# Kernel optimization log

Measured on AMD Instinct MI355X. Metric: run time of the kernel, lower is better.

## Reference

```python
import jax, jax.numpy as jnp
import numpy as np

D_MODEL = 512
NUM_HEADS = 8
HEAD_DIM = D_MODEL // NUM_HEADS
NUM_RBF = 16
MAX_DIST = 2.0
SCALE = HEAD_DIM ** -0.5
SIGMA = MAX_DIST / NUM_RBF


def setup_inputs() -> dict:
    key = jax.random.key(0)
    ks = jax.random.split(key, 8)
    B, L = 4, 1024
    x = jax.random.normal(ks[0], (B, L, D_MODEL), dtype=jnp.float32)
    coords = jax.random.normal(ks[1], (B, L, 3), dtype=jnp.float32)
    mask = jnp.ones((B, L), dtype=bool)
    # torch Linear weights stored transposed: (in, out)
    s = 1.0 / np.sqrt(D_MODEL)
    Wqkv = jax.random.uniform(ks[2], (D_MODEL, 3 * D_MODEL), jnp.float32, -s, s)
    bqkv = jax.random.uniform(ks[3], (3 * D_MODEL,), jnp.float32, -s, s)
    sr = 1.0 / np.sqrt(NUM_RBF)
    Wbias = jax.random.uniform(ks[4], (NUM_RBF, NUM_HEADS), jnp.float32, -sr, sr)
    bbias = jax.random.uniform(ks[5], (NUM_HEADS,), jnp.float32, -sr, sr)
    Wout = jax.random.uniform(ks[6], (D_MODEL, D_MODEL), jnp.float32, -s, s)
    bout = jax.random.uniform(ks[7], (D_MODEL,), jnp.float32, -s, s)
    return {"x": x, "coords": coords, "mask": mask,
            "Wqkv": Wqkv, "bqkv": bqkv, "Wbias": Wbias, "bbias": bbias,
            "Wout": Wout, "bout": bout}


def reference(x, coords, mask, Wqkv, bqkv, Wbias, bbias, Wout, bout):
    B, L, _ = x.shape
    qkv = x @ Wqkv + bqkv                              # (B,L,3*d)
    qkv = qkv.reshape(B, L, 3, NUM_HEADS, HEAD_DIM)
    qkv = jnp.transpose(qkv, (2, 0, 3, 1, 4))          # (3,B,H,L,hd)
    q, k, v = qkv[0], qkv[1], qkv[2]
    logits = jnp.einsum('bhqd,bhkd->bhqk', q, k) * SCALE
    # pairwise euclidean distances with safe sqrt (zero grad at d=0)
    diff = coords[:, :, None, :] - coords[:, None, :, :]  # (B,L,L,3)
    d2 = jnp.sum(diff * diff, axis=-1)
    dists = jnp.where(d2 > 0, jnp.sqrt(jnp.where(d2 > 0, d2, 1.0)), 0.0)
    mu = jnp.linspace(0.0, MAX_DIST, NUM_RBF)
    rbf = jnp.exp(-(dists[..., None] - mu) ** 2 / (2.0 * SIGMA ** 2))  # (B,L,L,R)
    geo = rbf @ Wbias + bbias                          # (B,L,L,H)
    logits = logits + jnp.transpose(geo, (0, 3, 1, 2))  # (B,H,L,L)
    neg_inf = jnp.finfo(logits.dtype).min
    logits = jnp.where(mask[:, None, None, :], logits, neg_inf)
    w = jax.nn.softmax(logits, axis=-1)
    out = jnp.einsum('bhqk,bhkd->bhqd', w, v)
    out = jnp.transpose(out, (0, 2, 1, 3)).reshape(B, L, D_MODEL)
    return out @ Wout + bout
```

## Files before the change

kernel.cpp:

```cpp
#include <hip/hip_runtime.h>
#include <hip/hip_bf16.h>

typedef unsigned short u16;
typedef unsigned int   u32;
typedef __attribute__((ext_vector_type(8))) __bf16 bf16x8;
typedef __attribute__((ext_vector_type(8))) unsigned short u16x8;
typedef __attribute__((ext_vector_type(4))) float  f32x4;

#define LOG2E 1.4426950408889634f
#define SC2   (0.125f * LOG2E)
#define NTAB  512
#define INV_DT128 21802.667f

__device__ __forceinline__ u16 f2bf(float f) {
  u32 u = __float_as_uint(f);
  u32 r = (u + 0x7FFFu + ((u >> 16) & 1u)) >> 16;
  return (u16)r;
}

__device__ __forceinline__ void gld16(const void* g, void* l) {
  __builtin_amdgcn_global_load_lds((const __attribute__((address_space(1))) void*)g,
                                   (__attribute__((address_space(3))) void*)l,
                                   16, 0, 0);
}

__device__ __forceinline__ int sigma64(int l) {
  return (l & ~0x3C) | ((l >> 2) & 0x0C) | ((l << 2) & 0x30);
}

__device__ __forceinline__ void tr64_body(const float* __restrict__ in, u16* __restrict__ out,
                                          int R, int C, int c0, int r0, int tid,
                                          float (*tile)[65]) {
  const int cl = tid & 63, rl = tid >> 6;
#pragma unroll
  for (int p = 0; p < 16; ++p) {
    int row = p * 4 + rl;
    tile[row][cl] = in[(size_t)(r0 + row) * C + c0 + cl];
  }
  __syncthreads();
#pragma unroll
  for (int p = 0; p < 16; ++p) {
    int cc = p * 4 + rl;
    out[(size_t)(c0 + cc) * R + r0 + cl] = f2bf(tile[cl][cc]);
  }
}

__global__ __launch_bounds__(256) void prep(
    const float* __restrict__ x, const float* __restrict__ Wqkv, const float* __restrict__ Wout,
    const float* __restrict__ Wbias, const float* __restrict__ bbias,
    const float* __restrict__ coords,
    u16* __restrict__ xb, u16* __restrict__ wqkvT, u16* __restrict__ woutT,
    u32* __restrict__ gpack, u16* __restrict__ didx) {
  __shared__ float tile[64][65];
  const int bx = blockIdx.x, tid = threadIdx.x;
  if (bx < 2048) {
    int i = bx * 256 + tid;
    float4 v = ((const float4*)x)[i];
    ushort4 o;
    o.x = f2bf(v.x); o.y = f2bf(v.y); o.z = f2bf(v.z); o.w = f2bf(v.w);
    ((ushort4*)xb)[i] = o;
  } else if (bx < 2240) {
    int t = bx - 2048;
    tr64_body(Wqkv, wqkvT, 512, 1536, (t % 24) * 64, (t / 24) * 64, tid, tile);
  } else if (bx < 2304) {
    int t = bx - 2240;
    tr64_body(Wout, woutT, 512, 512, (t & 7) * 64, (t >> 3) * 64, tid, tile);
  } else if (bx < 2306) {
    int i = (bx - 2304) * 256 + tid;
    float d0 = (float)i * (3.0f / 511.0f);
    float d1 = (float)(i + 1) * (3.0f / 511.0f);
    float g0[8], g1[8];
#pragma unroll
    for (int h = 0; h < 8; ++h) { g0[h] = bbias[h]; g1[h] = bbias[h]; }
#pragma unroll
    for (int r = 0; r < 16; ++r) {
      float mu = (float)r * (2.0f / 15.0f);
      float e0 = __expf(-(d0 - mu) * (d0 - mu) * 32.0f);
      float e1 = __expf(-(d1 - mu) * (d1 - mu) * 32.0f);
#pragma unroll
      for (int h = 0; h < 8; ++h) {
        g0[h] += e0 * Wbias[r * 8 + h];
        g1[h] += e1 * Wbias[r * 8 + h];
      }
    }
#pragma unroll
    for (int h = 0; h < 8; ++h) {
      u32 lo = f2bf(g0[h] * LOG2E);
      u32 hi = f2bf((g1[h] - g0[h]) * (LOG2E / 128.0f));
      gpack[h * NTAB + i] = (hi << 16) | lo;
    }
  } else {
    __shared__ float rcf[12];
    int bi = bx - 2306;
    int b = bi >> 8, it = bi & 255;
    int i0 = it * 4;
    if (tid < 12) rcf[tid] = coords[(size_t)b * 3072 + i0 * 3 + tid];
    __syncthreads();
#pragma unroll
    for (int jt = 0; jt < 4; ++jt) {
      int j = jt * 256 + tid;
      float cx = coords[((size_t)b * 1024 + j) * 3 + 0];
      float cy = coords[((size_t)b * 1024 + j) * 3 + 1];
      float cz = coords[((size_t)b * 1024 + j) * 3 + 2];
#pragma unroll
      for (int ii = 0; ii < 4; ++ii) {
        float dx = rcf[ii * 3 + 0] - cx, dy = rcf[ii * 3 + 1] - cy, dz = rcf[ii * 3 + 2] - cz;
        float d = sqrtf(fmaf(dx, dx, fmaf(dy, dy, dz * dz)));
        float t = fminf(d * INV_DT128, 65407.0f);
        didx[((size_t)b << 20) + (size_t)(i0 + ii) * 1024 + j] = (u16)(t + 0.5f);
      }
    }
  }
}

template <int EPI, int NT, int MT>
__global__ __launch_bounds__(256) void gemm_bt(
    const u16* __restrict__ A, const u16* __restrict__ Bt, const float* __restrict__ bias,
    float* __restrict__ Cf, u16* __restrict__ Qb, u16* __restrict__ Kb, u16* __restrict__ Vt,
    int N, int K) {
  __shared__ __attribute__((aligned(16))) u16 As[MT * 64 * 64];
  __shared__ __attribute__((aligned(16))) u16 Bs[NT * 16 * 64];
  const int tid = threadIdx.x;
  const int w = tid >> 6, lane = tid & 63;
  const int lm = lane & 15, lg = lane >> 4;
  const int m0 = blockIdx.y * (MT * 64), n0 = blockIdx.x * (NT * 16);
  const f32x4 z4 = {0.f, 0.f, 0.f, 0.f};
  f32x4 acc[MT][NT];
#pragma unroll
  for (int mt = 0; mt < MT; ++mt)
#pragma unroll
    for (int nt = 0; nt < NT; ++nt) acc[mt][nt] = z4;

  for (int k0 = 0; k0 < K; k0 += 64) {
    __syncthreads();
#pragma unroll
    for (int j = 0; j < 2 * MT; ++j) {
      int cidx = j * 256 + tid;
      int row = cidx >> 3, c8 = cidx & 7;
      gld16(A + (size_t)(m0 + row) * K + k0 + c8 * 8, &As[cidx * 8]);
    }
#pragma unroll
    for (int j = 0; j < NT / 2; ++j) {
      int cidx = j * 256 + tid;
      int row = cidx >> 3, c8 = cidx & 7;
      gld16(Bt + (size_t)(n0 + row) * K + k0 + c8 * 8, &Bs[cidx * 8]);
    }
    __syncthreads();
#pragma unroll
    for (int c = 0; c < 2; ++c) {
      const int ko = c * 32 + lg * 8;
      bf16x8 af[MT], bfr[NT];
#pragma unroll
      for (int mt = 0; mt < MT; ++mt)
        af[mt] = *(const bf16x8*)&As[(w * (MT * 16) + mt * 16 + lm) * 64 + ko];
#pragma unroll
      for (int nt = 0; nt < NT; ++nt)
        bfr[nt] = *(const bf16x8*)&Bs[(nt * 16 + lm) * 64 + ko];
#pragma unroll
      for (int mt = 0; mt < MT; ++mt)
#pragma unroll
        for (int nt = 0; nt < NT; ++nt)
          acc[mt][nt] = __builtin_amdgcn_mfma_f32_16x16x32_bf16(af[mt], bfr[nt], acc[mt][nt], 0, 0, 0);
    }
  }

#pragma unroll
  for (int mt = 0; mt < MT; ++mt) {
#pragma unroll
    for (int nt = 0; nt < NT; ++nt) {
      const int n = n0 + nt * 16 + lm;
      const float bv = bias[n];
#pragma unroll
      for (int r = 0; r < 4; ++r) {
        const int m = m0 + w * (MT * 16) + mt * 16 + lg * 4 + r;
        float v = acc[mt][nt][r] + bv;
        if (EPI == 1) {
          Cf[(size_t)m * N + n] = v;
        } else {
          int b = m >> 10, l = m & 1023;
          int which = n >> 9, f = n & 511, h = f >> 6, o = f & 63;
          u16 hv = f2bf(v);
          int lp = (l & ~63) | sigma64(l & 63);
          if (which == 0)      Qb[(((size_t)(b * 8 + h)) * 1024 + l) * 64 + o] = hv;
          else if (which == 1) Kb[(((size_t)(b * 8 + h)) * 1024 + lp) * 64 + o] = hv;
          else                 Vt[(((size_t)(b * 8 + h)) * 64 + o) * 1024 + lp] = hv;
        }
      }
    }
  }
}

__global__ __launch_bounds__(128, 4) void attn_kernel(
    const u16* __restrict__ Qb, const u16* __restrict__ Kb, const u16* __restrict__ Vt,
    const u16* __restrict__ didx, const u32* __restrict__ gpack, u16* __restrict__ Ob) {
  __shared__ __attribute__((aligned(16))) char smem[23040];
  u32* tab = (u32*)smem;
  u16* Ks = (u16*)(smem + 2048);
  u16* Vs = (u16*)(smem + 10240);

  const int tid = threadIdx.x;
  const int w = tid >> 6, lane = tid & 63;
  const int lm = lane & 15, lg = lane >> 4;
  const int bid = blockIdx.x;
  const int qt = bid & 31, bh = bid >> 5, h = bh & 7, b = bh >> 3;

  ((uint4*)tab)[tid] = ((const uint4*)(gpack + (size_t)h * NTAB))[tid];

  u16* Ps = (u16*)(smem + 18432 + w * 2304);

  const int qrow0 = qt * 32 + w * 16;
  bf16x8 qf[2];
  {
    const u16* qp = Qb + ((size_t)bh * 1024 + qrow0 + lm) * 64 + lg * 8;
    qf[0] = *(const bf16x8*)(qp);
    qf[1] = *(const bf16x8*)(qp + 32);
  }
  const u16* dptr = didx + ((size_t)b << 20) + (size_t)(qrow0 + lm) * 1024 + lg * 16;

  float l = 0.f;
  const f32x4 z4 = {0.f, 0.f, 0.f, 0.f};
  f32x4 Oacc[4];
#pragma unroll
  for (int ft = 0; ft < 4; ++ft) Oacc[ft] = z4;

  const int sw = lm & 7;

  for (int i = 0; i < 16; ++i) {
    __syncthreads();
#pragma unroll
    for (int j = 0; j < 4; ++j) {
      int cidx = j * 128 + tid;
      int row = cidx >> 3, c8s = (cidx & 7) ^ (row & 7);
      gld16(Kb + ((size_t)bh * 1024 + i * 64 + row) * 64 + c8s * 8, Ks + cidx * 8);
      gld16(Vt + ((size_t)bh * 64 + row) * 1024 + i * 64 + c8s * 8, Vs + cidx * 8);
    }
    u16x8 dv0 = *(const u16x8*)(dptr + i * 64);
    u16x8 dv1 = *(const u16x8*)(dptr + i * 64 + 8);
    __syncthreads();

    f32x4 S[4];
#pragma unroll
    for (int nt = 0; nt < 4; ++nt) S[nt] = z4;
#pragma unroll
    for (int c = 0; c < 2; ++c) {
#pragma unroll
      for (int nt = 0; nt < 4; ++nt) {
        bf16x8 kf = *(const bf16x8*)&Ks[(nt * 16 + lm) * 64 + (((c * 4 + lg) ^ sw) * 8)];
        S[nt] = __builtin_amdgcn_mfma_f32_16x16x32_bf16(kf, qf[c], S[nt], 0, 0, 0);
      }
    }
    float rs = 0.f;
#pragma unroll
    for (int nt = 0; nt < 4; ++nt)
#pragma unroll
      for (int r = 0; r < 4; ++r) {
        int t = nt * 4 + r;
        u32 u = (t < 8) ? (u32)dv0[t] : (u32)dv1[t - 8];
        u32 pk = tab[u >> 7];
        float fr = (float)(u & 127u);
        float g0 = __uint_as_float(pk << 16);
        float dg = __uint_as_float(pk & 0xffff0000u);
        float p = exp2f(fmaf(S[nt][r], SC2, fmaf(fr, dg, g0)));
        S[nt][r] = p;
        rs += p;
      }
    l += rs;
#pragma unroll
    for (int nt = 0; nt < 4; ++nt) {
      __hip_bfloat162 p01 = __float22bfloat162_rn(make_float2(S[nt][0], S[nt][1]));
      __hip_bfloat162 p23 = __float22bfloat162_rn(make_float2(S[nt][2], S[nt][3]));
      *(uint2*)&Ps[lm * 72 + nt * 16 + lg * 4] = make_uint2(*(u32*)&p01, *(u32*)&p23);
    }
    bf16x8 pa[2];
    pa[0] = *(const bf16x8*)&Ps[lm * 72 + lg * 8];
    pa[1] = *(const bf16x8*)&Ps[lm * 72 + 32 + lg * 8];
#pragma unroll
    for (int ft = 0; ft < 4; ++ft)
#pragma unroll
      for (int c = 0; c < 2; ++c) {
        bf16x8 vf = *(const bf16x8*)&Vs[(ft * 16 + lm) * 64 + (((c * 4 + lg) ^ sw) * 8)];
        Oacc[ft] = __builtin_amdgcn_mfma_f32_16x16x32_bf16(pa[c], vf, Oacc[ft], 0, 0, 0);
      }
  }

  l += __shfl_xor(l, 16);
  l += __shfl_xor(l, 32);
#pragma unroll
  for (int r = 0; r < 4; ++r) {
    float lr = __shfl(l, lg * 4 + r);
    float inv = 1.0f / lr;
    int qrow = qrow0 + lg * 4 + r;
    size_t o = ((size_t)b * 1024 + qrow) * 512 + h * 64;
#pragma unroll
    for (int ft = 0; ft < 4; ++ft)
      Ob[o + ft * 16 + lm] = f2bf(Oacc[ft][r] * inv);
  }
}

extern "C" void kernel_launch(void* const* d_in, const int* in_sizes, int n_in,
                              void* d_out, int out_size, void* d_ws, size_t ws_size,
                              hipStream_t stream) {
  const float* x      = (const float*)d_in[0];
  const float* coords = (const float*)d_in[1];
  const float* Wqkv   = (const float*)d_in[3];
  const float* bqkv   = (const float*)d_in[4];
  const float* Wbias  = (const float*)d_in[5];
  const float* bbias  = (const float*)d_in[6];
  const float* Wout   = (const float*)d_in[7];
  const float* bout   = (const float*)d_in[8];
  float* out = (float*)d_out;

  char* ws = (char*)d_ws;
  u16* xb     = (u16*)(ws + 0);
  u16* wqkvT  = (u16*)(ws + 4194304);
  u16* woutT  = (u16*)(ws + 5767168);
  u32* gpack  = (u32*)(ws + 6291456);
  u16* didx   = (u16*)(ws + 8388608);
  u16* qb     = (u16*)(ws + 16777216);
  u16* kb     = (u16*)(ws + 20971520);
  u16* vtb    = (u16*)(ws + 25165824);
  u16* attnb  = (u16*)(ws + 29360128);

  prep<<<3330, 256, 0, stream>>>(x, Wqkv, Wout, Wbias, bbias, coords,
                                 xb, wqkvT, woutT, gpack, didx);
  gemm_bt<0, 4, 2><<<dim3(24, 32), 256, 0, stream>>>(xb, wqkvT, bqkv, nullptr, qb, kb, vtb, 1536, 512);
  attn_kernel<<<1024, 128, 0, stream>>>(qb, kb, vtb, didx, gpack, attnb);
  gemm_bt<1, 4, 1><<<dim3(8, 64), 256, 0, stream>>>(attnb, woutT, bout, out, nullptr, nullptr, nullptr, 512, 512);
}
```

Baseline: 145.3 us.

## Split attention over key halves with atomic fp32 partials and normalize in out-projection

The attention kernel now handles 64 query rows per block with four waves and splits the keys into two halves. Each half adds its unnormalized output and row sums into fp32 buffers with atomics, which works because the softmax has no running max. A new out-projection GEMM reads those partials, divides by the summed denominators, converts to bf16 and multiplies by Wout. Block IDs are remapped for locality. This doubles the number of waves and shortens each wave's key loop, at the cost of a zeroing kernel, 8MB of atomic traffic and a workspace that now reuses the old xb/wqkvT region.

```diff
diff --git a/kernel.cpp b/kernel.cpp
--- a/kernel.cpp
+++ b/kernel.cpp
@@ -190,10 +190,15 @@
   }
 }
 
-__global__ __launch_bounds__(128, 4) void attn_kernel(
+__global__ __launch_bounds__(256) void zerok(float4* __restrict__ p) {
+  p[(size_t)blockIdx.x * 256 + threadIdx.x] = make_float4(0.f, 0.f, 0.f, 0.f);
+}
+
+__global__ __launch_bounds__(256, 4) void attn_kernel(
     const u16* __restrict__ Qb, const u16* __restrict__ Kb, const u16* __restrict__ Vt,
-    const u16* __restrict__ didx, const u32* __restrict__ gpack, u16* __restrict__ Ob) {
-  __shared__ __attribute__((aligned(16))) char smem[23040];
+    const u16* __restrict__ didx, const u32* __restrict__ gpack,
+    float* __restrict__ Op, float* __restrict__ lp) {
+  __shared__ __attribute__((aligned(16))) char smem[27648];
   u32* tab = (u32*)smem;
   u16* Ks = (u16*)(smem + 2048);
   u16* Vs = (u16*)(smem + 10240);
@@ -201,38 +206,39 @@
   const int tid = threadIdx.x;
   const int w = tid >> 6, lane = tid & 63;
   const int lm = lane & 15, lg = lane >> 4;
-  const int bid = blockIdx.x;
-  const int qt = bid & 31, bh = bid >> 5, h = bh & 7, b = bh >> 3;
-
-  ((uint4*)tab)[tid] = ((const uint4*)(gpack + (size_t)h * NTAB))[tid];
+  const int bid = (blockIdx.x & 7) * 128 + (blockIdx.x >> 3);
+  const int qt = bid & 15, sp = (bid >> 4) & 1, bh = bid >> 5, h = bh & 7, b = bh >> 3;
+
+  ((uint2*)tab)[tid] = ((const uint2*)(gpack + (size_t)h * NTAB))[tid];
 
   u16* Ps = (u16*)(smem + 18432 + w * 2304);
 
-  const int qrow0 = qt * 32 + w * 16;
+  const int qrow0 = qt * 64 + w * 16;
   bf16x8 qf[2];
   {
     const u16* qp = Qb + ((size_t)bh * 1024 + qrow0 + lm) * 64 + lg * 8;
     qf[0] = *(const bf16x8*)(qp);
     qf[1] = *(const bf16x8*)(qp + 32);
   }
-  const u16* dptr = didx + ((size_t)b << 20) + (size_t)(qrow0 + lm) * 1024 + lg * 16;
+  const int kb0 = sp * 512;
+  const u16* dptr = didx + ((size_t)b << 20) + (size_t)(qrow0 + lm) * 1024 + kb0 + lg * 16;
 
   float l = 0.f;
   const f32x4 z4 = {0.f, 0.f, 0.f, 0.f};
-  f32x4 Oacc[4];
-#pragma unroll
-  for (int ft = 0; ft < 4; ++ft) Oacc[ft] = z4;
+  f32x4 Oa[4];
+#pragma unroll
+  for (int ft = 0; ft < 4; ++ft) Oa[ft] = z4;
 
   const int sw = lm & 7;
 
-  for (int i = 0; i < 16; ++i) {
-    __syncthreads();
-#pragma unroll
-    for (int j = 0; j < 4; ++j) {
-      int cidx = j * 128 + tid;
+  for (int i = 0; i < 8; ++i) {
+    __syncthreads();
+#pragma unroll
+    for (int j = 0; j < 2; ++j) {
+      int cidx = j * 256 + tid;
       int row = cidx >> 3, c8s = (cidx & 7) ^ (row & 7);
-      gld16(Kb + ((size_t)bh * 1024 + i * 64 + row) * 64 + c8s * 8, Ks + cidx * 8);
-      gld16(Vt + ((size_t)bh * 64 + row) * 1024 + i * 64 + c8s * 8, Vs + cidx * 8);
+      gld16(Kb + ((size_t)bh * 1024 + kb0 + i * 64 + row) * 64 + c8s * 8, Ks + cidx * 8);
+      gld16(Vt + ((size_t)bh * 64 + row) * 1024 + kb0 + i * 64 + c8s * 8, Vs + cidx * 8);
     }
     u16x8 dv0 = *(const u16x8*)(dptr + i * 64);
     u16x8 dv1 = *(const u16x8*)(dptr + i * 64 + 8);
@@ -279,7 +285,8 @@
 #pragma unroll
       for (int c = 0; c < 2; ++c) {
         bf16x8 vf = *(const bf16x8*)&Vs[(ft * 16 + lm) * 64 + (((c * 4 + lg) ^ sw) * 8)];
-        Oacc[ft] = __builtin_amdgcn_mfma_f32_16x16x32_bf16(pa[c], vf, Oacc[ft], 0, 0, 0);
+        Oacc_helper: ;
+        Oa[ft] = __builtin_amdgcn_mfma_f32_16x16x32_bf16(pa[c], vf, Oa[ft], 0, 0, 0);
       }
   }
 
@@ -287,13 +294,84 @@
   l += __shfl_xor(l, 32);
 #pragma unroll
   for (int r = 0; r < 4; ++r) {
-    float lr = __shfl(l, lg * 4 + r);
-    float inv = 1.0f / lr;
     int qrow = qrow0 + lg * 4 + r;
-    size_t o = ((size_t)b * 1024 + qrow) * 512 + h * 64;
+    size_t o = ((size_t)bh * 1024 + qrow) * 64;
 #pragma unroll
     for (int ft = 0; ft < 4; ++ft)
-      Ob[o + ft * 16 + lm] = f2bf(Oacc[ft][r] * inv);
+      unsafeAtomicAdd(&Op[o + ft * 16 + lm], Oa[ft][r]);
+  }
+  if (lg == 0) unsafeAtomicAdd(&lp[(size_t)bh * 1024 + qrow0 + lm], l);
+}
+
+__global__ __launch_bounds__(256) void gemm_out(
+    const float* __restrict__ Op, const float* __restrict__ lp,
+    const u16* __restrict__ Bt, const float* __restrict__ bias, float* __restrict__ Cf) {
+  __shared__ __attribute__((aligned(16))) u16 As[64 * 64];
+  __shared__ __attribute__((aligned(16))) u16 Bs[64 * 64];
+  const int tid = threadIdx.x;
+  const int w = tid >> 6, lane = tid & 63;
+  const int lm = lane & 15, lg = lane >> 4;
+  const int m0 = blockIdx.y * 64, n0 = blockIdx.x * 64;
+  const f32x4 z4 = {0.f, 0.f, 0.f, 0.f};
+  f32x4 acc[4];
+#pragma unroll
+  for (int nt = 0; nt < 4; ++nt) acc[nt] = z4;
+
+  const int arow = tid >> 2, aseg = tid & 3;
+  const int am = m0 + arow, ab = am >> 10, al = am & 1023;
+
+  for (int k0 = 0; k0 < 512; k0 += 64) {
+    const int h = k0 >> 6;
+    __syncthreads();
+#pragma unroll
+    for (int j = 0; j < 2; ++j) {
+      int cidx = j * 256 + tid;
+      int row = cidx >> 3, c8 = cidx & 7;
+      gld16(Bt + (size_t)(n0 + row) * 512 + k0 + c8 * 8, &Bs[cidx * 8]);
+    }
+    {
+      const size_t rb = ((size_t)(ab * 8 + h)) * 1024 + al;
+      const float* src = Op + rb * 64 + aseg * 16;
+      const float inv = 1.0f / lp[rb];
+      f32x4 v0 = *(const f32x4*)(src + 0);
+      f32x4 v1 = *(const f32x4*)(src + 4);
+      f32x4 v2 = *(const f32x4*)(src + 8);
+      f32x4 v3 = *(const f32x4*)(src + 12);
+      union { u16 us[16]; uint4 q[2]; } t;
+#pragma unroll
+      for (int j = 0; j < 4; ++j) {
+        t.us[j]      = f2bf(v0[j] * inv);
+        t.us[4 + j]  = f2bf(v1[j] * inv);
+        t.us[8 + j]  = f2bf(v2[j] * inv);
+        t.us[12 + j] = f2bf(v3[j] * inv);
+      }
+      const int rs = arow & 7;
+      *(uint4*)&As[arow * 64 + (((aseg * 2) ^ rs) * 8)]     = t.q[0];
+      *(uint4*)&As[arow * 64 + (((aseg * 2 + 1) ^ rs) * 8)] = t.q[1];
+    }
+    __syncthreads();
+#pragma unroll
+    for (int c = 0; c < 2; ++c) {
+      const int ko = c * 32 + lg * 8;
+      bf16x8 af = *(const bf16x8*)&As[(w * 16 + lm) * 64 + (((c * 4 + lg) ^ (lm & 7)) * 8)];
+      bf16x8 bfr[4];
+#pragma unroll
+      for (int nt = 0; nt < 4; ++nt)
+        bfr[nt] = *(const bf16x8*)&Bs[(nt * 16 + lm) * 64 + ko];
+#pragma unroll
+      for (int nt = 0; nt < 4; ++nt)
+        acc[nt] = __builtin_amdgcn_mfma_f32_16x16x32_bf16(af, bfr[nt], acc[nt], 0, 0, 0);
+    }
+  }
+#pragma unroll
+  for (int nt = 0; nt < 4; ++nt) {
+    const int n = n0 + nt * 16 + lm;
+    const float bv = bias[n];
+#pragma unroll
+    for (int r = 0; r < 4; ++r) {
+      const int m = m0 + w * 16 + lg * 4 + r;
+      Cf[(size_t)m * 512 + n] = acc[nt][r] + bv;
+    }
   }
 }
 
@@ -311,19 +389,21 @@
   float* out = (float*)d_out;
 
   char* ws = (char*)d_ws;
-  u16* xb     = (u16*)(ws + 0);
-  u16* wqkvT  = (u16*)(ws + 4194304);
-  u16* woutT  = (u16*)(ws + 5767168);
-  u32* gpack  = (u32*)(ws + 6291456);
-  u16* didx   = (u16*)(ws + 8388608);
-  u16* qb     = (u16*)(ws + 16777216);
-  u16* kb     = (u16*)(ws + 20971520);
-  u16* vtb    = (u16*)(ws + 25165824);
-  u16* attnb  = (u16*)(ws + 29360128);
+  u16*   xb    = (u16*)(ws + 0);
+  u16*   wqkvT = (u16*)(ws + 0x400000);
+  float* Op    = (float*)(ws + 0);
+  float* lpb   = (float*)(ws + 0x800000);
+  u16* woutT = (u16*)(ws + 0x820000);
+  u32* gpack = (u32*)(ws + 0x8A0000);
+  u16* didx  = (u16*)(ws + 0x8A4000);
+  u16* qb    = (u16*)(ws + 0x10A4000);
+  u16* kb    = (u16*)(ws + 0x14A4000);
+  u16* vtb   = (u16*)(ws + 0x18A4000);
 
   prep<<<3330, 256, 0, stream>>>(x, Wqkv, Wout, Wbias, bbias, coords,
                                  xb, wqkvT, woutT, gpack, didx);
   gemm_bt<0, 4, 2><<<dim3(24, 32), 256, 0, stream>>>(xb, wqkvT, bqkv, nullptr, qb, kb, vtb, 1536, 512);
-  attn_kernel<<<1024, 128, 0, stream>>>(qb, kb, vtb, didx, gpack, attnb);
-  gemm_bt<1, 4, 1><<<dim3(8, 64), 256, 0, stream>>>(attnb, woutT, bout, out, nullptr, nullptr, nullptr, 512, 512);
-}
+  zerok<<<2080, 256, 0, stream>>>((float4*)ws);
+  attn_kernel<<<1024, 256, 0, stream>>>(qb, kb, vtb, didx, gpack, Op, lpb);
+  gemm_out<<<dim3(8, 64), 256, 0, stream>>>(Op, lpb, woutT, bout, out);
+}
```

Result: slower. 152.7 us (+5.1%).

## Split attention key range across two wave groups with LDS reduction

Applied to the files above, without the earlier changes.

The attention kernel now runs 512-thread blocks covering 64 query rows, with two halves of four waves each processing half of the key sequence (split-K). Partial output accumulators and row sums from the second half are combined through LDS before normalization and the store. Blocks are remapped so consecutive block indices spread across heads, and each K/V tile is shared by four waves instead of two. The change aims to raise K/V reuse and halve the sequential loop length per wave, at the cost of a larger LDS footprint, an extra reduction step, and half the waves idle during the epilogue.

```diff
diff --git a/kernel.cpp b/kernel.cpp
--- a/kernel.cpp
+++ b/kernel.cpp
@@ -190,49 +190,52 @@
   }
 }
 
-__global__ __launch_bounds__(128, 4) void attn_kernel(
+__global__ __launch_bounds__(512, 4) void attn_kernel(
     const u16* __restrict__ Qb, const u16* __restrict__ Kb, const u16* __restrict__ Vt,
     const u16* __restrict__ didx, const u32* __restrict__ gpack, u16* __restrict__ Ob) {
-  __shared__ __attribute__((aligned(16))) char smem[23040];
+  __shared__ __attribute__((aligned(16))) char smem[53248];
   u32* tab = (u32*)smem;
-  u16* Ks = (u16*)(smem + 2048);
-  u16* Vs = (u16*)(smem + 10240);
 
   const int tid = threadIdx.x;
   const int w = tid >> 6, lane = tid & 63;
   const int lm = lane & 15, lg = lane >> 4;
-  const int bid = blockIdx.x;
-  const int qt = bid & 31, bh = bid >> 5, h = bh & 7, b = bh >> 3;
-
-  ((uint4*)tab)[tid] = ((const uint4*)(gpack + (size_t)h * NTAB))[tid];
-
-  u16* Ps = (u16*)(smem + 18432 + w * 2304);
-
-  const int qrow0 = qt * 32 + w * 16;
+  const int half = w >> 2, wq = w & 3;
+  const int bid = (blockIdx.x & 7) * 64 + (blockIdx.x >> 3);
+  const int qt = bid & 15, bh = bid >> 4, h = bh & 7, b = bh >> 3;
+
+  u16* Ks = (u16*)(smem + 2048 + half * 16384);
+  u16* Vs = (u16*)(smem + 10240 + half * 16384);
+  u16* Ps = (u16*)(smem + 34816 + w * 2304);
+
+  tab[tid] = gpack[(size_t)h * NTAB + tid];
+
+  const int qrow0 = qt * 64 + wq * 16;
   bf16x8 qf[2];
   {
     const u16* qp = Qb + ((size_t)bh * 1024 + qrow0 + lm) * 64 + lg * 8;
     qf[0] = *(const bf16x8*)(qp);
     qf[1] = *(const bf16x8*)(qp + 32);
   }
-  const u16* dptr = didx + ((size_t)b << 20) + (size_t)(qrow0 + lm) * 1024 + lg * 16;
+  const int kb0 = half * 512;
+  const u16* dptr = didx + ((size_t)b << 20) + (size_t)(qrow0 + lm) * 1024 + kb0 + lg * 16;
 
   float l = 0.f;
   const f32x4 z4 = {0.f, 0.f, 0.f, 0.f};
-  f32x4 Oacc[4];
-#pragma unroll
-  for (int ft = 0; ft < 4; ++ft) Oacc[ft] = z4;
+  f32x4 Oa[4];
+#pragma unroll
+  for (int ft = 0; ft < 4; ++ft) Oa[ft] = z4;
 
   const int sw = lm & 7;
-
-  for (int i = 0; i < 16; ++i) {
-    __syncthreads();
-#pragma unroll
-    for (int j = 0; j < 4; ++j) {
-      int cidx = j * 128 + tid;
+  const int htid = tid & 255;
+
+  for (int i = 0; i < 8; ++i) {
+    __syncthreads();
+#pragma unroll
+    for (int j = 0; j < 2; ++j) {
+      int cidx = j * 256 + htid;
       int row = cidx >> 3, c8s = (cidx & 7) ^ (row & 7);
-      gld16(Kb + ((size_t)bh * 1024 + i * 64 + row) * 64 + c8s * 8, Ks + cidx * 8);
-      gld16(Vt + ((size_t)bh * 64 + row) * 1024 + i * 64 + c8s * 8, Vs + cidx * 8);
+      gld16(Kb + ((size_t)bh * 1024 + kb0 + i * 64 + row) * 64 + c8s * 8, Ks + cidx * 8);
+      gld16(Vt + ((size_t)bh * 64 + row) * 1024 + kb0 + i * 64 + c8s * 8, Vs + cidx * 8);
     }
     u16x8 dv0 = *(const u16x8*)(dptr + i * 64);
     u16x8 dv1 = *(const u16x8*)(dptr + i * 64 + 8);
@@ -279,21 +282,39 @@
 #pragma unroll
       for (int c = 0; c < 2; ++c) {
         bf16x8 vf = *(const bf16x8*)&Vs[(ft * 16 + lm) * 64 + (((c * 4 + lg) ^ sw) * 8)];
-        Oacc[ft] = __builtin_amdgcn_mfma_f32_16x16x32_bf16(pa[c], vf, Oacc[ft], 0, 0, 0);
+        Oa[ft] = __builtin_amdgcn_mfma_f32_16x16x32_bf16(pa[c], vf, Oa[ft], 0, 0, 0);
       }
   }
 
   l += __shfl_xor(l, 16);
   l += __shfl_xor(l, 32);
-#pragma unroll
-  for (int r = 0; r < 4; ++r) {
-    float lr = __shfl(l, lg * 4 + r);
-    float inv = 1.0f / lr;
-    int qrow = qrow0 + lg * 4 + r;
-    size_t o = ((size_t)b * 1024 + qrow) * 512 + h * 64;
+
+  __syncthreads();
+  float* mO = (float*)(smem + 2048);
+  float* mL = (float*)(smem + 18432);
+  if (half == 1) {
 #pragma unroll
     for (int ft = 0; ft < 4; ++ft)
-      Ob[o + ft * 16 + lm] = f2bf(Oacc[ft][r] * inv);
+#pragma unroll
+      for (int r = 0; r < 4; ++r)
+        mO[wq * 1024 + (lg * 4 + r) * 64 + ft * 16 + lm] = Oa[ft][r];
+    if (lg == 0) mL[wq * 16 + lm] = l;
+  }
+  __syncthreads();
+  if (half == 0) {
+    l += mL[wq * 16 + lm];
+#pragma unroll
+    for (int r = 0; r < 4; ++r) {
+      float lr = __shfl(l, lg * 4 + r);
+      float inv = 1.0f / lr;
+      int qrow = qrow0 + lg * 4 + r;
+      size_t o = ((size_t)b * 1024 + qrow) * 512 + h * 64;
+#pragma unroll
+      for (int ft = 0; ft < 4; ++ft) {
+        float vsum = Oa[ft][r] + mO[wq * 1024 + (lg * 4 + r) * 64 + ft * 16 + lm];
+        Ob[o + ft * 16 + lm] = f2bf(vsum * inv);
+      }
+    }
   }
 }
 
@@ -324,6 +345,6 @@
   prep<<<3330, 256, 0, stream>>>(x, Wqkv, Wout, Wbias, bbias, coords,
                                  xb, wqkvT, woutT, gpack, didx);
   gemm_bt<0, 4, 2><<<dim3(24, 32), 256, 0, stream>>>(xb, wqkvT, bqkv, nullptr, qb, kb, vtb, 1536, 512);
-  attn_kernel<<<1024, 128, 0, stream>>>(qb, kb, vtb, didx, gpack, attnb);
+  attn_kernel<<<512, 512, 0, stream>>>(qb, kb, vtb, didx, gpack, attnb);
   gemm_bt<1, 4, 1><<<dim3(8, 64), 256, 0, stream>>>(attnb, woutT, bout, out, nullptr, nullptr, nullptr, 512, 512);
 }
```

New measurement: 138.2 us. -4.9%, faster.
